# Optimization experiments

Hardware: AMD Instinct MI355X
Metric: run time of the kernel (lower is better)

## Reference

```python
import jax, jax.numpy as jnp
import numpy as np

OUTPUT_SEQ_LEN = 64


def setup_inputs() -> dict:
    key = jax.random.key(0)
    ks = jax.random.split(key, 12)
    S, B, H, O = 256, 256, 512, 64  # src_len, batch, hidden, output vocab
    sos_token = jax.random.normal(ks[0], (1, B, O), dtype=jnp.float32)
    h = jax.random.normal(ks[1], (1, B, H), dtype=jnp.float32)
    encoder_outputs = jax.random.normal(ks[2], (S, B, H), dtype=jnp.float32)
    s = 0.05
    params = {
        'Wa': jax.random.normal(ks[3], (2 * H, H), dtype=jnp.float32) * s,  # attn linear
        'ba': jnp.zeros((H,), dtype=jnp.float32),
        'v': jax.random.normal(ks[4], (H,), dtype=jnp.float32) * s,          # scoring vector
        'W_ih': jax.random.normal(ks[5], (H, O + H), dtype=jnp.float32) * s,
        'b_ih': jnp.zeros((H,), dtype=jnp.float32),
        'W_hh': jax.random.normal(ks[6], (H, H), dtype=jnp.float32) * s,
        'b_hh': jnp.zeros((H,), dtype=jnp.float32),
        'Wo': jax.random.normal(ks[7], (O, H), dtype=jnp.float32) * s,       # output linear
        'bo': jnp.zeros((O,), dtype=jnp.float32),
    }
    return {'sos_token': sos_token, 'h': h, 'encoder_outputs': encoder_outputs, **params}


def reference(sos_token, h, encoder_outputs, Wa, ba, v, W_ih, b_ih, W_hh, b_hh, Wo, bo):
    # predict=True path of Decoder.forward: greedy argmax feedback each step.
    O = sos_token.shape[-1]
    h0 = h[0]                      # [B, H]
    x0 = sos_token[0]              # [B, O]

    def step(carry, _):
        h_t, x_t = carry           # [B,H], [B,O]
        # Bahdanau attention: score over source positions (softmax over dim 0)
        hid = jnp.broadcast_to(h_t[None], encoder_outputs.shape)          # [S,B,H]
        energy = jnp.tanh(jnp.concatenate([hid, encoder_outputs], axis=2) @ Wa + ba)  # [S,B,H]
        score = energy @ v                                                # [S,B]
        attn = jax.nn.softmax(score, axis=0)                              # [S,B]
        context = jnp.einsum('sb,sbh->bh', attn, encoder_outputs)         # [B,H]
        # single-layer vanilla RNN cell
        rnn_in = jnp.concatenate([x_t, context], axis=1)                  # [B,O+H]
        h_new = jnp.tanh(rnn_in @ W_ih.T + b_ih + h_t @ W_hh.T + b_hh)    # [B,H]
        out = h_new @ Wo.T + bo                                           # [B,O]
        # greedy feedback: one_hot(argmax(softmax(out))) == one_hot(argmax(out))
        x_next = jax.nn.one_hot(jnp.argmax(out, axis=1), O, dtype=out.dtype)
        return (h_new, x_next), out

    _, outs = jax.lax.scan(step, (h0, x0), None, length=OUTPUT_SEQ_LEN)   # [T,B,O]
    preds = outs[: OUTPUT_SEQ_LEN - 1]                                    # [T-1,B,O]
    preds = jnp.transpose(preds, (1, 2, 0))                               # [B,O,T-1]
    return preds
```

## Files before the change

### kernel.cpp

```cpp
#include <hip/hip_runtime.h>
#include <math.h>

#define SS 256
#define BB 256
#define HH 512
#define OO 64
#define NSTEP 63

__device__ __forceinline__ float fast_tanh(float x) {
    float e = __builtin_amdgcn_exp2f(x * 2.885390081777927f);
    return 1.f - 2.f * __builtin_amdgcn_rcpf(e + 1.f);
}

__global__ __launch_bounds__(256) void k_ew_gemm(const float* __restrict__ A,
                                                 const float* __restrict__ Bm,
                                                 float* __restrict__ C)
{
    __shared__ float As[8][132];
    __shared__ float Bs[8][132];
    const int tid = threadIdx.x;
    const int bm = blockIdx.x * 128;
    const int bn = blockIdx.y * 128;
    const int tx = tid & 15;
    const int ty = tid >> 4;
    const int a_row = tid >> 1;
    const int a_k4 = (tid & 1) * 4;
    const int b_row = tid >> 5;
    const int b_n4 = (tid & 31) * 4;

    float acc[8][8];
#pragma unroll
    for (int i = 0; i < 8; i++)
#pragma unroll
        for (int j = 0; j < 8; j++) acc[i][j] = 0.f;

    for (int kt = 0; kt < 512; kt += 8) {
        float4 av = *(const float4*)(A + (size_t)(bm + a_row) * 512 + kt + a_k4);
        As[a_k4 + 0][a_row] = av.x;
        As[a_k4 + 1][a_row] = av.y;
        As[a_k4 + 2][a_row] = av.z;
        As[a_k4 + 3][a_row] = av.w;
        *(float4*)(&Bs[b_row][b_n4]) = *(const float4*)(Bm + (size_t)(kt + b_row) * 512 + bn + b_n4);
        __syncthreads();
#pragma unroll
        for (int kk = 0; kk < 8; kk++) {
            float av8[8], bv8[8];
            *(float4*)&av8[0] = *(const float4*)&As[kk][ty * 4];
            *(float4*)&av8[4] = *(const float4*)&As[kk][64 + ty * 4];
            *(float4*)&bv8[0] = *(const float4*)&Bs[kk][tx * 4];
            *(float4*)&bv8[4] = *(const float4*)&Bs[kk][64 + tx * 4];
#pragma unroll
            for (int i = 0; i < 8; i++)
#pragma unroll
                for (int j = 0; j < 8; j++) acc[i][j] += av8[i] * bv8[j];
        }
        __syncthreads();
    }
#pragma unroll
    for (int i = 0; i < 8; i++) {
        int m = bm + ((i < 4) ? (ty * 4 + i) : (64 + ty * 4 + i - 4));
        int mrow = (m & 255) * 256 + (m >> 8);
        float4 o0 = make_float4(acc[i][0], acc[i][1], acc[i][2], acc[i][3]);
        float4 o1 = make_float4(acc[i][4], acc[i][5], acc[i][6], acc[i][7]);
        *(float4*)(C + (size_t)mrow * 512 + bn + tx * 4) = o0;
        *(float4*)(C + (size_t)mrow * 512 + bn + 64 + tx * 4) = o1;
    }
}

__global__ __launch_bounds__(256) void k_qinit(const float* __restrict__ A,
                                               const float* __restrict__ Wa,
                                               float* __restrict__ qpre)
{
    __shared__ float As[32][33];
    __shared__ float Bs[32][33];
    const int tid = threadIdx.x;
    const int bn = blockIdx.x * 32;
    const int bm = blockIdx.y * 32;
    const int tx = tid & 15;
    const int ty = tid >> 4;
    const int l_row = tid >> 3;
    const int l_c4 = (tid & 7) * 4;

    float acc00 = 0.f, acc01 = 0.f, acc10 = 0.f, acc11 = 0.f;
    for (int kt = 0; kt < 512; kt += 32) {
#pragma unroll
        for (int i = 0; i < 4; i++)
            As[l_c4 + i][l_row] = A[(size_t)(bm + l_row) * 512 + kt + l_c4 + i];
#pragma unroll
        for (int i = 0; i < 4; i++)
            Bs[l_row][l_c4 + i] = Wa[(size_t)(kt + l_row) * 512 + bn + l_c4 + i];
        __syncthreads();
#pragma unroll
        for (int kk = 0; kk < 32; kk++) {
            float a0 = As[kk][ty * 2], a1 = As[kk][ty * 2 + 1];
            float b0 = Bs[kk][tx * 2], b1 = Bs[kk][tx * 2 + 1];
            acc00 += a0 * b0; acc01 += a0 * b1;
            acc10 += a1 * b0; acc11 += a1 * b1;
        }
        __syncthreads();
    }
    qpre[(size_t)(bm + ty * 2) * 512 + bn + tx * 2]     = acc00;
    qpre[(size_t)(bm + ty * 2) * 512 + bn + tx * 2 + 1] = acc01;
    qpre[(size_t)(bm + ty * 2 + 1) * 512 + bn + tx * 2]     = acc10;
    qpre[(size_t)(bm + ty * 2 + 1) * 512 + bn + tx * 2 + 1] = acc11;
}

__global__ __launch_bounds__(1024) void k_attn(const float* __restrict__ EW,
                                               const float* __restrict__ enc,
                                               const float* __restrict__ qpre,
                                               const float* __restrict__ ba,
                                               const float* __restrict__ vvec,
                                               float* __restrict__ ctx,
                                               float* __restrict__ hpre_out,
                                               const float* __restrict__ ob,
                                               const float* __restrict__ bo,
                                               float* __restrict__ dout,
                                               float* __restrict__ xb,
                                               int t)
{
    __shared__ float qs[512];
    __shared__ float vs[512];
    __shared__ float sc[256];
    __shared__ float red[16];
    __shared__ float ctxp[16][512];
    const int b = blockIdx.x;
    const int tid = threadIdx.x;

    if (t > 0 && tid < 64) {
        const int l = tid;
        float v = ob[b * 64 + l] + bo[l];
        dout[(size_t)b * (OO * NSTEP) + l * NSTEP + (t - 1)] = v;
        int bi = l;
        float bv = v;
#pragma unroll
        for (int off = 1; off < 64; off <<= 1) {
            float ov = __shfl_xor(bv, off);
            int oi = __shfl_xor(bi, off);
            if (ov > bv || (ov == bv && oi < bi)) { bv = ov; bi = oi; }
        }
        xb[b * 64 + l] = (l == bi) ? 1.0f : 0.0f;
    }

    if (tid < 576) {
        int idx = b * 576 + tid;
        if (idx < 131072) hpre_out[idx] = 0.f;
    }

    if (tid < 512) {
        qs[tid] = qpre[b * 512 + tid] + ba[tid];
        vs[tid] = vvec[tid];
    }
    __syncthreads();

    const int w = tid >> 6;
    const int l = tid & 63;

    float qv[8], vv[8];
    *(float4*)&qv[0] = *(const float4*)&qs[l * 8];
    *(float4*)&qv[4] = *(const float4*)&qs[l * 8 + 4];
    *(float4*)&vv[0] = *(const float4*)&vs[l * 8];
    *(float4*)&vv[4] = *(const float4*)&vs[l * 8 + 4];

    {
        const float4* pe = (const float4*)(EW + ((size_t)b * 256 + w * 16) * 512);
        for (int i = 0; i < 16; i += 2) {
            float4 e00 = pe[(size_t)i * 128 + 2 * l];
            float4 e01 = pe[(size_t)i * 128 + 2 * l + 1];
            float4 e10 = pe[(size_t)(i + 1) * 128 + 2 * l];
            float4 e11 = pe[(size_t)(i + 1) * 128 + 2 * l + 1];
            float a0, a1;
            a0  = vv[0] * fast_tanh(e00.x + qv[0]);
            a0 += vv[1] * fast_tanh(e00.y + qv[1]);
            a0 += vv[2] * fast_tanh(e00.z + qv[2]);
            a0 += vv[3] * fast_tanh(e00.w + qv[3]);
            a0 += vv[4] * fast_tanh(e01.x + qv[4]);
            a0 += vv[5] * fast_tanh(e01.y + qv[5]);
            a0 += vv[6] * fast_tanh(e01.z + qv[6]);
            a0 += vv[7] * fast_tanh(e01.w + qv[7]);
            a1  = vv[0] * fast_tanh(e10.x + qv[0]);
            a1 += vv[1] * fast_tanh(e10.y + qv[1]);
            a1 += vv[2] * fast_tanh(e10.z + qv[2]);
            a1 += vv[3] * fast_tanh(e10.w + qv[3]);
            a1 += vv[4] * fast_tanh(e11.x + qv[4]);
            a1 += vv[5] * fast_tanh(e11.y + qv[5]);
            a1 += vv[6] * fast_tanh(e11.z + qv[6]);
            a1 += vv[7] * fast_tanh(e11.w + qv[7]);
#pragma unroll
            for (int off = 32; off; off >>= 1) {
                a0 += __shfl_down(a0, off);
                a1 += __shfl_down(a1, off);
            }
            if (l == 0) {
                sc[w * 16 + i]     = a0;
                sc[w * 16 + i + 1] = a1;
            }
        }
    }
    __syncthreads();

    if (tid < 256) {
        float m = sc[tid];
#pragma unroll
        for (int off = 32; off; off >>= 1) m = fmaxf(m, __shfl_down(m, off));
        if ((tid & 63) == 0) red[tid >> 6] = m;
    }
    __syncthreads();
    if (tid < 256) {
        float mx = fmaxf(fmaxf(red[0], red[1]), fmaxf(red[2], red[3]));
        float e = expf(sc[tid] - mx);
        sc[tid] = e;
        float ssum = e;
#pragma unroll
        for (int off = 32; off; off >>= 1) ssum += __shfl_down(ssum, off);
        if ((tid & 63) == 0) red[8 + (tid >> 6)] = ssum;
    }
    __syncthreads();
    const float inv = 1.0f / (red[8] + red[9] + red[10] + red[11]);

    {
        float c[8];
#pragma unroll
        for (int j = 0; j < 8; j++) c[j] = 0.f;
        for (int i = 0; i < 16; i += 2) {
            int s0 = w * 16 + i;
            int s1 = s0 + 1;
            float w0 = sc[s0];
            float w1 = sc[s1];
            const float4* p0 = (const float4*)(enc + ((size_t)s0 * 256 + b) * 512);
            const float4* p1 = (const float4*)(enc + ((size_t)s1 * 256 + b) * 512);
            float4 e00 = p0[2 * l];
            float4 e01 = p0[2 * l + 1];
            float4 e10 = p1[2 * l];
            float4 e11 = p1[2 * l + 1];
            c[0] += w0 * e00.x; c[1] += w0 * e00.y;
            c[2] += w0 * e00.z; c[3] += w0 * e00.w;
            c[4] += w0 * e01.x; c[5] += w0 * e01.y;
            c[6] += w0 * e01.z; c[7] += w0 * e01.w;
            c[0] += w1 * e10.x; c[1] += w1 * e10.y;
            c[2] += w1 * e10.z; c[3] += w1 * e10.w;
            c[4] += w1 * e11.x; c[5] += w1 * e11.y;
            c[6] += w1 * e11.z; c[7] += w1 * e11.w;
        }
        float4 c0 = make_float4(c[0], c[1], c[2], c[3]);
        float4 c1 = make_float4(c[4], c[5], c[6], c[7]);
        *(float4*)&ctxp[w][l * 8]     = c0;
        *(float4*)&ctxp[w][l * 8 + 4] = c1;
    }
    __syncthreads();
    if (tid < 512) {
        float r = 0.f;
#pragma unroll
        for (int g = 0; g < 16; g++) r += ctxp[g][tid];
        ctx[b * 512 + tid] = r * inv;
    }
}

__global__ __launch_bounds__(256) void k_h(
    const float* __restrict__ xin, const float* __restrict__ ctx,
    const float* __restrict__ hpre_in, const float* __restrict__ h0,
    int t0,
    const float* __restrict__ W_ih, const float* __restrict__ W_hh,
    const float* __restrict__ b_ih, const float* __restrict__ b_hh,
    float* __restrict__ hpre_out, float* __restrict__ qpre,
    float* __restrict__ ob)
{
    __shared__ float As[8][34];
    __shared__ float Bs[8][68];
    const int tid = threadIdx.x;
    const int bn = blockIdx.x * 64;
    const int bm = blockIdx.y * 32;
    const int k0 = blockIdx.z * 136;

    {
        int lin = ((blockIdx.z * 8 + blockIdx.y) * 8 + blockIdx.x) * 256 + tid;
        qpre[lin] = 0.f;
    }
    if (blockIdx.z == 7) {
        int lin = (blockIdx.y * 8 + blockIdx.x) * 256 + tid;
        ob[lin] = 0.f;
    }

    const int tx = tid & 15;
    const int ty = tid >> 4;
    const int sa_k = tid & 7;
    const int sa_m = tid >> 3;
    const int sb_n = tid >> 2;
    const int sb_k = (tid & 3) * 2;

    float acc[2][4];
#pragma unroll
    for (int i = 0; i < 2; i++)
#pragma unroll
        for (int j = 0; j < 4; j++) acc[i][j] = 0.f;

    for (int kt = 0; kt < 17; kt++) {
        const int kb = k0 + kt * 8;
        {
            int m = bm + sa_m;
            int k = kb + sa_k;
            float v;
            if (k < 64) v = xin[m * 64 + k];
            else if (k < 576) v = ctx[m * 512 + (k - 64)];
            else {
                int kh = k - 576;
                v = t0 ? h0[m * 512 + kh]
                       : tanhf(hpre_in[m * 512 + kh] + b_ih[kh] + b_hh[kh]);
            }
            As[sa_k][sa_m] = v;
        }
        {
            int n = bn + sb_n;
#pragma unroll
            for (int i = 0; i < 2; i++) {
                int k = kb + sb_k + i;
                float v = (k < 576) ? W_ih[(size_t)n * 576 + k]
                                    : W_hh[(size_t)n * 512 + (k - 576)];
                Bs[sb_k + i][sb_n] = v;
            }
        }
        __syncthreads();
#pragma unroll
        for (int kk = 0; kk < 8; kk++) {
            float a0 = As[kk][ty * 2], a1 = As[kk][ty * 2 + 1];
            float b0 = Bs[kk][tx * 4], b1 = Bs[kk][tx * 4 + 1];
            float b2 = Bs[kk][tx * 4 + 2], b3 = Bs[kk][tx * 4 + 3];
            acc[0][0] += a0 * b0; acc[0][1] += a0 * b1;
            acc[0][2] += a0 * b2; acc[0][3] += a0 * b3;
            acc[1][0] += a1 * b0; acc[1][1] += a1 * b1;
            acc[1][2] += a1 * b2; acc[1][3] += a1 * b3;
        }
        __syncthreads();
    }
#pragma unroll
    for (int i = 0; i < 2; i++) {
        int m = bm + ty * 2 + i;
#pragma unroll
        for (int j = 0; j < 4; j++) {
            atomicAdd(&hpre_out[(size_t)m * 512 + bn + tx * 4 + j], acc[i][j]);
        }
    }
}

__global__ __launch_bounds__(256) void k_outq(
    const float* __restrict__ hpre_cur,
    const float* __restrict__ b_ih, const float* __restrict__ b_hh,
    const float* __restrict__ Wo, const float* __restrict__ Wa,
    float* __restrict__ ob, float* __restrict__ qpre)
{
    __shared__ float As[8][34];
    __shared__ float Bs[8][68];
    const int tid = threadIdx.x;
    const int bn = blockIdx.x * 64;
    const int bm = blockIdx.y * 32;
    const int k0 = blockIdx.z * 128;
    const bool is_out = (bn < 64);

    const int tx = tid & 15;
    const int ty = tid >> 4;
    const int sa_k = tid & 7;
    const int sa_m = tid >> 3;
    const int sb_n = tid >> 2;
    const int sb_k = (tid & 3) * 2;
    const int qa_k = tid >> 5;
    const int qa_n = (tid & 31) * 2;

    float acc[2][4];
#pragma unroll
    for (int i = 0; i < 2; i++)
#pragma unroll
        for (int j = 0; j < 4; j++) acc[i][j] = 0.f;

    for (int kt = 0; kt < 16; kt++) {
        const int kb = k0 + kt * 8;
        {
            int m = bm + sa_m;
            int k = kb + sa_k;
            As[sa_k][sa_m] = tanhf(hpre_cur[(size_t)m * 512 + k] + b_ih[k] + b_hh[k]);
        }
        if (is_out) {
            int n = bn + sb_n;
#pragma unroll
            for (int i = 0; i < 2; i++) {
                int k = kb + sb_k + i;
                Bs[sb_k + i][sb_n] = Wo[(size_t)n * 512 + k];
            }
        } else {
            int k = kb + qa_k;
            int n = bn - 64 + qa_n;
#pragma unroll
            for (int i = 0; i < 2; i++)
                Bs[qa_k][qa_n + i] = Wa[(size_t)k * 512 + n + i];
        }
        __syncthreads();
#pragma unroll
        for (int kk = 0; kk < 8; kk++) {
            float a0 = As[kk][ty * 2], a1 = As[kk][ty * 2 + 1];
            float b0 = Bs[kk][tx * 4], b1 = Bs[kk][tx * 4 + 1];
            float b2 = Bs[kk][tx * 4 + 2], b3 = Bs[kk][tx * 4 + 3];
            acc[0][0] += a0 * b0; acc[0][1] += a0 * b1;
            acc[0][2] += a0 * b2; acc[0][3] += a0 * b3;
            acc[1][0] += a1 * b0; acc[1][1] += a1 * b1;
            acc[1][2] += a1 * b2; acc[1][3] += a1 * b3;
        }
        __syncthreads();
    }
#pragma unroll
    for (int i = 0; i < 2; i++) {
        int m = bm + ty * 2 + i;
#pragma unroll
        for (int j = 0; j < 4; j++) {
            int n = bn + tx * 4 + j;
            if (is_out) atomicAdd(&ob[m * 64 + n], acc[i][j]);
            else        atomicAdd(&qpre[(size_t)m * 512 + (n - 64)], acc[i][j]);
        }
    }
}

__global__ __launch_bounds__(256) void k_argmax(const float* __restrict__ ob,
                                                const float* __restrict__ bo,
                                                float* __restrict__ dout, int t,
                                                float* __restrict__ x)
{
    const int b = blockIdx.x * 4 + (threadIdx.x >> 6);
    const int l = threadIdx.x & 63;
    float v = ob[b * 64 + l] + bo[l];
    dout[(size_t)b * (OO * NSTEP) + l * NSTEP + t] = v;
    int bi = l;
    float bv = v;
#pragma unroll
    for (int off = 1; off < 64; off <<= 1) {
        float ov = __shfl_xor(bv, off);
        int oi = __shfl_xor(bi, off);
        if (ov > bv || (ov == bv && oi < bi)) { bv = ov; bi = oi; }
    }
    x[b * 64 + l] = (l == bi) ? 1.0f : 0.0f;
}

extern "C" void kernel_launch(void* const* d_in, const int* in_sizes, int n_in,
                              void* d_out, int out_size, void* d_ws, size_t ws_size,
                              hipStream_t stream)
{
    const float* sos  = (const float*)d_in[0];
    const float* h0   = (const float*)d_in[1];
    const float* enc  = (const float*)d_in[2];
    const float* Wa   = (const float*)d_in[3];
    const float* ba   = (const float*)d_in[4];
    const float* vvec = (const float*)d_in[5];
    const float* W_ih = (const float*)d_in[6];
    const float* b_ih = (const float*)d_in[7];
    const float* W_hh = (const float*)d_in[8];
    const float* b_hh = (const float*)d_in[9];
    const float* Wo   = (const float*)d_in[10];
    const float* bo   = (const float*)d_in[11];
    float* out = (float*)d_out;

    float* ws = (float*)d_ws;
    float* EW    = ws; ws += (size_t)SS * BB * HH;
    float* qpre  = ws; ws += BB * HH;
    float* ctx   = ws; ws += BB * HH;
    float* hpre0 = ws; ws += BB * HH;
    float* hpre1 = ws; ws += BB * HH;
    float* xb    = ws; ws += BB * OO;
    float* ob    = ws; ws += BB * OO;

    k_ew_gemm<<<dim3(512, 4), 256, 0, stream>>>(enc, Wa + 512 * 512, EW);
    k_qinit<<<dim3(16, 8), 256, 0, stream>>>(h0, Wa, qpre);

    for (int t = 0; t < NSTEP; t++) {
        float* hpre_out = (t & 1) ? hpre1 : hpre0;
        float* hpre_in  = (t & 1) ? hpre0 : hpre1;
        const float* xin = (t == 0) ? sos : xb;

        k_attn<<<256, 1024, 0, stream>>>(EW, enc, qpre, ba, vvec, ctx,
                                         hpre_out, ob, bo, out, xb, t);

        k_h<<<dim3(8, 8, 8), 256, 0, stream>>>(xin, ctx, hpre_in, h0, (t == 0) ? 1 : 0,
                                               W_ih, W_hh, b_ih, b_hh,
                                               hpre_out, qpre, ob);

        k_outq<<<dim3(9, 8, 4), 256, 0, stream>>>(hpre_out, b_ih, b_hh,
                                                  Wo, Wa, ob, qpre);
    }

    k_argmax<<<64, 256, 0, stream>>>(ob, bo, out, NSTEP - 1, xb);
}
```

Before: 6.730 ms.

## Replace split-K atomics in RNN and output GEMMs with full-K tiles and fused tanh

The hidden-state and output/query GEMMs drop split-K and atomicAdd accumulation. Each block now covers the whole K range with 32-wide k tiles and float4 weight loads. Tanh plus bias is applied once in k_h's epilogue, so h is stored directly and the zero-init writes spread across kernels go away. This removes atomic traffic, buffer clearing and repeated tanh work. The cost is fewer blocks (256 and 144) with a long serial K loop, so each GEMM has less parallelism.

```diff
diff --git a/kernel.cpp b/kernel.cpp
--- a/kernel.cpp
+++ b/kernel.cpp
@@ -111,7 +111,6 @@
                                                const float* __restrict__ ba,
                                                const float* __restrict__ vvec,
                                                float* __restrict__ ctx,
-                                               float* __restrict__ hpre_out,
                                                const float* __restrict__ ob,
                                                const float* __restrict__ bo,
                                                float* __restrict__ dout,
@@ -139,11 +138,6 @@
             if (ov > bv || (ov == bv && oi < bi)) { bv = ov; bi = oi; }
         }
         xb[b * 64 + l] = (l == bi) ? 1.0f : 0.0f;
-    }
-
-    if (tid < 576) {
-        int idx = b * 576 + tid;
-        if (idx < 131072) hpre_out[idx] = 0.f;
     }
 
     if (tid < 512) {
@@ -257,162 +251,137 @@
 
 __global__ __launch_bounds__(256) void k_h(
     const float* __restrict__ xin, const float* __restrict__ ctx,
-    const float* __restrict__ hpre_in, const float* __restrict__ h0,
-    int t0,
+    const float* __restrict__ hprev,
     const float* __restrict__ W_ih, const float* __restrict__ W_hh,
     const float* __restrict__ b_ih, const float* __restrict__ b_hh,
-    float* __restrict__ hpre_out, float* __restrict__ qpre,
-    float* __restrict__ ob)
-{
-    __shared__ float As[8][34];
-    __shared__ float Bs[8][68];
+    float* __restrict__ hout)
+{
+    __shared__ float As[32][17];
+    __shared__ float Bs[32][33];
     const int tid = threadIdx.x;
-    const int bn = blockIdx.x * 64;
-    const int bm = blockIdx.y * 32;
-    const int k0 = blockIdx.z * 136;
-
-    {
-        int lin = ((blockIdx.z * 8 + blockIdx.y) * 8 + blockIdx.x) * 256 + tid;
-        qpre[lin] = 0.f;
-    }
-    if (blockIdx.z == 7) {
-        int lin = (blockIdx.y * 8 + blockIdx.x) * 256 + tid;
-        ob[lin] = 0.f;
-    }
-
-    const int tx = tid & 15;
-    const int ty = tid >> 4;
-    const int sa_k = tid & 7;
-    const int sa_m = tid >> 3;
-    const int sb_n = tid >> 2;
-    const int sb_k = (tid & 3) * 2;
-
-    float acc[2][4];
-#pragma unroll
-    for (int i = 0; i < 2; i++)
-#pragma unroll
-        for (int j = 0; j < 4; j++) acc[i][j] = 0.f;
-
-    for (int kt = 0; kt < 17; kt++) {
-        const int kb = k0 + kt * 8;
-        {
-            int m = bm + sa_m;
-            int k = kb + sa_k;
+    const int bn = blockIdx.x * 32;
+    const int bm = blockIdx.y * 16;
+
+    const int tx = tid & 31;
+    const int ty = tid >> 5;
+    const int sa_m = tid >> 5;
+    const int sa_k = tid & 31;
+    const int sb_n = tid >> 3;
+    const int sb_k4 = (tid & 7) * 4;
+
+    float acc0 = 0.f, acc1 = 0.f;
+
+    for (int kt = 0; kt < 34; kt++) {
+        const int k0 = kt * 32;
+#pragma unroll
+        for (int it = 0; it < 2; it++) {
+            int m = bm + sa_m + it * 8;
+            int k = k0 + sa_k;
             float v;
             if (k < 64) v = xin[m * 64 + k];
             else if (k < 576) v = ctx[m * 512 + (k - 64)];
-            else {
-                int kh = k - 576;
-                v = t0 ? h0[m * 512 + kh]
-                       : tanhf(hpre_in[m * 512 + kh] + b_ih[kh] + b_hh[kh]);
-            }
-            As[sa_k][sa_m] = v;
+            else v = hprev[m * 512 + (k - 576)];
+            As[sa_k][sa_m + it * 8] = v;
         }
         {
             int n = bn + sb_n;
-#pragma unroll
-            for (int i = 0; i < 2; i++) {
-                int k = kb + sb_k + i;
-                float v = (k < 576) ? W_ih[(size_t)n * 576 + k]
-                                    : W_hh[(size_t)n * 512 + (k - 576)];
-                Bs[sb_k + i][sb_n] = v;
-            }
-        }
-        __syncthreads();
-#pragma unroll
-        for (int kk = 0; kk < 8; kk++) {
-            float a0 = As[kk][ty * 2], a1 = As[kk][ty * 2 + 1];
-            float b0 = Bs[kk][tx * 4], b1 = Bs[kk][tx * 4 + 1];
-            float b2 = Bs[kk][tx * 4 + 2], b3 = Bs[kk][tx * 4 + 3];
-            acc[0][0] += a0 * b0; acc[0][1] += a0 * b1;
-            acc[0][2] += a0 * b2; acc[0][3] += a0 * b3;
-            acc[1][0] += a1 * b0; acc[1][1] += a1 * b1;
-            acc[1][2] += a1 * b2; acc[1][3] += a1 * b3;
-        }
-        __syncthreads();
-    }
-#pragma unroll
-    for (int i = 0; i < 2; i++) {
-        int m = bm + ty * 2 + i;
-#pragma unroll
-        for (int j = 0; j < 4; j++) {
-            atomicAdd(&hpre_out[(size_t)m * 512 + bn + tx * 4 + j], acc[i][j]);
-        }
+            int k = k0 + sb_k4;
+            float4 v4;
+            if (k < 576) v4 = *(const float4*)(W_ih + (size_t)n * 576 + k);
+            else         v4 = *(const float4*)(W_hh + (size_t)n * 512 + (k - 576));
+            Bs[sb_k4 + 0][sb_n] = v4.x;
+            Bs[sb_k4 + 1][sb_n] = v4.y;
+            Bs[sb_k4 + 2][sb_n] = v4.z;
+            Bs[sb_k4 + 3][sb_n] = v4.w;
+        }
+        __syncthreads();
+#pragma unroll
+        for (int kk = 0; kk < 32; kk++) {
+            float b = Bs[kk][tx];
+            acc0 += As[kk][ty * 2] * b;
+            acc1 += As[kk][ty * 2 + 1] * b;
+        }
+        __syncthreads();
+    }
+    {
+        int n = bn + tx;
+        float bias = b_ih[n] + b_hh[n];
+        int m0 = bm + ty * 2;
+        hout[(size_t)m0 * 512 + n]       = tanhf(acc0 + bias);
+        hout[(size_t)(m0 + 1) * 512 + n] = tanhf(acc1 + bias);
     }
 }
 
 __global__ __launch_bounds__(256) void k_outq(
-    const float* __restrict__ hpre_cur,
-    const float* __restrict__ b_ih, const float* __restrict__ b_hh,
+    const float* __restrict__ h,
     const float* __restrict__ Wo, const float* __restrict__ Wa,
     float* __restrict__ ob, float* __restrict__ qpre)
 {
-    __shared__ float As[8][34];
-    __shared__ float Bs[8][68];
+    __shared__ float As[32][17];
+    __shared__ float Bs[32][65];
     const int tid = threadIdx.x;
     const int bn = blockIdx.x * 64;
-    const int bm = blockIdx.y * 32;
-    const int k0 = blockIdx.z * 128;
-    const bool is_out = (bn < 64);
-
-    const int tx = tid & 15;
-    const int ty = tid >> 4;
-    const int sa_k = tid & 7;
-    const int sa_m = tid >> 3;
-    const int sb_n = tid >> 2;
-    const int sb_k = (tid & 3) * 2;
-    const int qa_k = tid >> 5;
-    const int qa_n = (tid & 31) * 2;
-
-    float acc[2][4];
-#pragma unroll
-    for (int i = 0; i < 2; i++)
-#pragma unroll
-        for (int j = 0; j < 4; j++) acc[i][j] = 0.f;
+    const int bm = blockIdx.y * 16;
+    const bool is_out = (bn == 0);
+
+    const int tx = tid & 63;
+    const int ty = tid >> 6;
+    const int sa_m = tid >> 5;
+    const int sa_k = tid & 31;
+    const int wo_n = tid >> 2;
+    const int wo_k8 = (tid & 3) * 8;
+    const int wa_k = tid >> 3;
+    const int wa_n8 = (tid & 7) * 8;
+
+    float acc[4] = {0.f, 0.f, 0.f, 0.f};
 
     for (int kt = 0; kt < 16; kt++) {
-        const int kb = k0 + kt * 8;
-        {
-            int m = bm + sa_m;
-            int k = kb + sa_k;
-            As[sa_k][sa_m] = tanhf(hpre_cur[(size_t)m * 512 + k] + b_ih[k] + b_hh[k]);
+        const int k0 = kt * 32;
+#pragma unroll
+        for (int it = 0; it < 2; it++) {
+            int m = bm + sa_m + it * 8;
+            As[sa_k][sa_m + it * 8] = h[(size_t)m * 512 + k0 + sa_k];
         }
         if (is_out) {
-            int n = bn + sb_n;
-#pragma unroll
-            for (int i = 0; i < 2; i++) {
-                int k = kb + sb_k + i;
-                Bs[sb_k + i][sb_n] = Wo[(size_t)n * 512 + k];
-            }
+            float4 v0 = *(const float4*)(Wo + (size_t)wo_n * 512 + k0 + wo_k8);
+            float4 v1 = *(const float4*)(Wo + (size_t)wo_n * 512 + k0 + wo_k8 + 4);
+            Bs[wo_k8 + 0][wo_n] = v0.x;
+            Bs[wo_k8 + 1][wo_n] = v0.y;
+            Bs[wo_k8 + 2][wo_n] = v0.z;
+            Bs[wo_k8 + 3][wo_n] = v0.w;
+            Bs[wo_k8 + 4][wo_n] = v1.x;
+            Bs[wo_k8 + 5][wo_n] = v1.y;
+            Bs[wo_k8 + 6][wo_n] = v1.z;
+            Bs[wo_k8 + 7][wo_n] = v1.w;
         } else {
-            int k = kb + qa_k;
-            int n = bn - 64 + qa_n;
-#pragma unroll
-            for (int i = 0; i < 2; i++)
-                Bs[qa_k][qa_n + i] = Wa[(size_t)k * 512 + n + i];
-        }
-        __syncthreads();
-#pragma unroll
-        for (int kk = 0; kk < 8; kk++) {
-            float a0 = As[kk][ty * 2], a1 = As[kk][ty * 2 + 1];
-            float b0 = Bs[kk][tx * 4], b1 = Bs[kk][tx * 4 + 1];
-            float b2 = Bs[kk][tx * 4 + 2], b3 = Bs[kk][tx * 4 + 3];
-            acc[0][0] += a0 * b0; acc[0][1] += a0 * b1;
-            acc[0][2] += a0 * b2; acc[0][3] += a0 * b3;
-            acc[1][0] += a1 * b0; acc[1][1] += a1 * b1;
-            acc[1][2] += a1 * b2; acc[1][3] += a1 * b3;
-        }
-        __syncthreads();
-    }
-#pragma unroll
-    for (int i = 0; i < 2; i++) {
-        int m = bm + ty * 2 + i;
-#pragma unroll
-        for (int j = 0; j < 4; j++) {
-            int n = bn + tx * 4 + j;
-            if (is_out) atomicAdd(&ob[m * 64 + n], acc[i][j]);
-            else        atomicAdd(&qpre[(size_t)m * 512 + (n - 64)], acc[i][j]);
-        }
+            const float* wp = Wa + (size_t)(k0 + wa_k) * 512 + (bn - 64) + wa_n8;
+            float4 v0 = *(const float4*)(wp);
+            float4 v1 = *(const float4*)(wp + 4);
+            Bs[wa_k][wa_n8 + 0] = v0.x;
+            Bs[wa_k][wa_n8 + 1] = v0.y;
+            Bs[wa_k][wa_n8 + 2] = v0.z;
+            Bs[wa_k][wa_n8 + 3] = v0.w;
+            Bs[wa_k][wa_n8 + 4] = v1.x;
+            Bs[wa_k][wa_n8 + 5] = v1.y;
+            Bs[wa_k][wa_n8 + 6] = v1.z;
+            Bs[wa_k][wa_n8 + 7] = v1.w;
+        }
+        __syncthreads();
+#pragma unroll
+        for (int kk = 0; kk < 32; kk++) {
+            float b = Bs[kk][tx];
+            acc[0] += As[kk][ty * 4 + 0] * b;
+            acc[1] += As[kk][ty * 4 + 1] * b;
+            acc[2] += As[kk][ty * 4 + 2] * b;
+            acc[3] += As[kk][ty * 4 + 3] * b;
+        }
+        __syncthreads();
+    }
+#pragma unroll
+    for (int i = 0; i < 4; i++) {
+        int m = bm + ty * 4 + i;
+        if (is_out) ob[m * 64 + tx] = acc[i];
+        else        qpre[(size_t)m * 512 + (bn - 64) + tx] = acc[i];
     }
 }
 
@@ -455,31 +424,29 @@
     float* out = (float*)d_out;
 
     float* ws = (float*)d_ws;
-    float* EW    = ws; ws += (size_t)SS * BB * HH;
-    float* qpre  = ws; ws += BB * HH;
-    float* ctx   = ws; ws += BB * HH;
-    float* hpre0 = ws; ws += BB * HH;
-    float* hpre1 = ws; ws += BB * HH;
-    float* xb    = ws; ws += BB * OO;
-    float* ob    = ws; ws += BB * OO;
+    float* EW   = ws; ws += (size_t)SS * BB * HH;
+    float* qpre = ws; ws += BB * HH;
+    float* ctx  = ws; ws += BB * HH;
+    float* hb0  = ws; ws += BB * HH;
+    float* hb1  = ws; ws += BB * HH;
+    float* xb   = ws; ws += BB * OO;
+    float* ob   = ws; ws += BB * OO;
 
     k_ew_gemm<<<dim3(512, 4), 256, 0, stream>>>(enc, Wa + 512 * 512, EW);
     k_qinit<<<dim3(16, 8), 256, 0, stream>>>(h0, Wa, qpre);
 
     for (int t = 0; t < NSTEP; t++) {
-        float* hpre_out = (t & 1) ? hpre1 : hpre0;
-        float* hpre_in  = (t & 1) ? hpre0 : hpre1;
+        const float* hprev = (t == 0) ? h0 : ((t & 1) ? hb0 : hb1);
+        float* hcur = (t & 1) ? hb1 : hb0;
         const float* xin = (t == 0) ? sos : xb;
 
         k_attn<<<256, 1024, 0, stream>>>(EW, enc, qpre, ba, vvec, ctx,
-                                         hpre_out, ob, bo, out, xb, t);
-
-        k_h<<<dim3(8, 8, 8), 256, 0, stream>>>(xin, ctx, hpre_in, h0, (t == 0) ? 1 : 0,
-                                               W_ih, W_hh, b_ih, b_hh,
-                                               hpre_out, qpre, ob);
-
-        k_outq<<<dim3(9, 8, 4), 256, 0, stream>>>(hpre_out, b_ih, b_hh,
-                                                  Wo, Wa, ob, qpre);
+                                         ob, bo, out, xb, t);
+
+        k_h<<<dim3(16, 16), 256, 0, stream>>>(xin, ctx, hprev,
+                                              W_ih, W_hh, b_ih, b_hh, hcur);
+
+        k_outq<<<dim3(9, 16), 256, 0, stream>>>(hcur, Wo, Wa, ob, qpre);
     }
 
     k_argmax<<<64, 256, 0, stream>>>(ob, bo, out, NSTEP - 1, xb);
```

Measured after the change: 9.200 ms. 36.7% more time.
